# Kernel optimization log

Measured on AMD Instinct MI355X. Metric: run time of the kernel, lower is better.

## Reference

```python
import jax, jax.numpy as jnp
import numpy as np

DIM = 512
NUM_HEADS = 8
HEAD_DIM = DIM // NUM_HEADS


def setup_inputs() -> dict:
    key = jax.random.key(0)
    ks = jax.random.split(key, 5)
    s = 0.02
    x = jax.random.normal(ks[0], (2, 4096, DIM), dtype=jnp.float32)
    W_qkv = jax.random.normal(ks[1], (DIM, 3 * DIM), dtype=jnp.float32) * s
    b_qkv = jnp.zeros((3 * DIM,), dtype=jnp.float32)
    W_proj = jax.random.normal(ks[2], (DIM, DIM), dtype=jnp.float32) * s
    b_proj = jnp.zeros((DIM,), dtype=jnp.float32)
    return {"x": x, "W_qkv": W_qkv, "b_qkv": b_qkv, "W_proj": W_proj, "b_proj": b_proj}


def reference(x, W_qkv, b_qkv, W_proj, b_proj):
    B, N, C = x.shape
    # qkv: [B,N,3C] -> [3,B,H,N,Dh]
    qkv = (x @ W_qkv + b_qkv).reshape(B, N, 3, NUM_HEADS, HEAD_DIM)
    qkv = jnp.transpose(qkv, (2, 0, 3, 1, 4))
    q, k, v = qkv[0], qkv[1], qkv[2]
    scale = HEAD_DIM ** -0.5
    # naive full attention matrix [B,H,N,N] (faithful to source)
    attn = jnp.einsum('bhqd,bhkd->bhqk', q, k) * scale
    attn = jax.nn.softmax(attn, axis=-1)
    out = jnp.einsum('bhqk,bhkd->bhqd', attn, v)  # [B,H,N,Dh]
    out = jnp.transpose(out, (0, 2, 1, 3)).reshape(B, N, C)
    return out @ W_proj + b_proj
```

## Files before the change

kernel.cpp:

```cpp
#include <hip/hip_runtime.h>
#include <stdint.h>

typedef _Float16 f16;
typedef _Float16 f16x4 __attribute__((ext_vector_type(4)));
typedef _Float16 f16x8 __attribute__((ext_vector_type(8)));
typedef float f32x4 __attribute__((ext_vector_type(4)));
typedef float f32x16 __attribute__((ext_vector_type(16)));
typedef uint32_t u32;
typedef u32 u32x2 __attribute__((ext_vector_type(2)));
typedef u32 u32x4 __attribute__((ext_vector_type(4)));

#define NHEADS 8
#define DH 64
#define BATCH 2
#define SEQ 4096
#define CDIM 512
#define MTOT (BATCH * SEQ)
#define QSCALE 0.18033688011112042f

__device__ __forceinline__ void gload_lds16(const void* g, void* l) {
  __builtin_amdgcn_global_load_lds(
      (const __attribute__((address_space(1))) uint32_t*)g,
      (__attribute__((address_space(3))) uint32_t*)l, 16, 0, 0);
}

__device__ __forceinline__ u32 pk2(float a, float b) {
  auto h = __builtin_amdgcn_cvt_pkrtz(a, b);
  return __builtin_bit_cast(u32, h);
}

__device__ __forceinline__ void pl32swap(u32& a, u32& b) {
  asm volatile("v_permlane32_swap_b32 %0, %1" : "+v"(a), "+v"(b));
}

__device__ __forceinline__ void tr64(const float* __restrict__ src,
                                     f16* __restrict__ dst, int k0, int n0,
                                     int Ns, int Ks, f16* L) {
  const int t = threadIdx.x;
#pragma unroll
  for (int i = 0; i < 8; ++i) {
    int idx = (i * 256 + t) * 2;
    int r = idx >> 6, c = idx & 63;
    float2 v = *(const float2*)(src + (size_t)(k0 + r) * Ns + n0 + c);
    L[c * 66 + r] = (f16)v.x;
    L[(c + 1) * 66 + r] = (f16)v.y;
  }
  __syncthreads();
#pragma unroll
  for (int i = 0; i < 8; ++i) {
    int idx = (i * 256 + t) * 2;
    int r = idx >> 6, c = idx & 63;
    *(u32*)(dst + (size_t)(n0 + r) * Ks + k0 + c) = *(const u32*)(L + r * 66 + c);
  }
}

__global__ void prep(const float* __restrict__ x, f16* __restrict__ xb,
                     const float* __restrict__ Wqkv, f16* __restrict__ wqkvT,
                     const float* __restrict__ Wproj, f16* __restrict__ wprojT) {
  __shared__ f16 L[64 * 66];
  const int b = blockIdx.x;
  if (b < 4096) {
    int i = (b * 256 + (int)threadIdx.x) * 4;
    float4 v = *(const float4*)(x + i);
    f16x4 o = {(f16)v.x, (f16)v.y, (f16)v.z, (f16)v.w};
    *(f16x4*)(xb + i) = o;
  } else if (b < 4096 + 192) {
    int tw = b - 4096;
    int kt = tw / 24, nt = tw % 24;
    tr64(Wqkv, wqkvT, kt << 6, nt << 6, 1536, 512, L);
  } else {
    int tw = b - 4096 - 192;
    int kt = tw >> 3, nt = tw & 7;
    tr64(Wproj, wprojT, kt << 6, nt << 6, 512, 512, L);
  }
}

template <int MODE>
__global__ __launch_bounds__(256) void gemm_f16(
    const f16* __restrict__ A, const f16* __restrict__ Bt,
    const float* __restrict__ bias, int Ncols,
    f16* __restrict__ Qo, f16* __restrict__ Ko, f16* __restrict__ Vo,
    float* __restrict__ Fo) {
  const int K = CDIM;
  const int nTN = Ncols >> 7;
  const int cpx = gridDim.x >> 3;
  const int vb = (blockIdx.x & 7) * cpx + (blockIdx.x >> 3);
  const int bm = vb / nTN, bn = vb % nTN;
  const int M0 = bm << 7, N0 = bn << 7;
  __shared__ __align__(16) char ldsA[128 * 64 * 2];
  __shared__ __align__(16) char ldsB[128 * 64 * 2];
  const int t = threadIdx.x;
  const int w = t >> 6, lane = t & 63;
  const int wr = w >> 1, wc = w & 1;
  const int lm = lane & 15, lk = lane >> 4;
  f32x4 acc[4][4] = {};

  const int srow = t >> 3;
  const int sj = t & 7;

  for (int k0 = 0; k0 < K; k0 += 64) {
    __syncthreads();
#pragma unroll
    for (int q = 0; q < 4; ++q) {
      int row = (q << 5) + srow;
      int col = (sj ^ (row & 7)) << 3;
      gload_lds16(A + (size_t)(M0 + row) * K + k0 + col,
                  ldsA + ((q << 8) + (w << 6)) * 16);
      gload_lds16(Bt + (size_t)(N0 + row) * K + k0 + col,
                  ldsB + ((q << 8) + (w << 6)) * 16);
    }
    asm volatile("s_waitcnt vmcnt(0)" ::: "memory");
    __syncthreads();
#pragma unroll
    for (int h = 0; h < 2; ++h) {
      f16x8 af[4], bf[4];
#pragma unroll
      for (int mi = 0; mi < 4; ++mi) {
        int row = (wr << 6) + (mi << 4) + lm;
        int slot = ((h << 2) + lk) ^ (row & 7);
        af[mi] = *(const f16x8*)(ldsA + row * 128 + slot * 16);
      }
#pragma unroll
      for (int ni = 0; ni < 4; ++ni) {
        int row = (wc << 6) + (ni << 4) + lm;
        int slot = ((h << 2) + lk) ^ (row & 7);
        bf[ni] = *(const f16x8*)(ldsB + row * 128 + slot * 16);
      }
#pragma unroll
      for (int mi = 0; mi < 4; ++mi)
#pragma unroll
        for (int ni = 0; ni < 4; ++ni)
          acc[mi][ni] = __builtin_amdgcn_mfma_f32_16x16x32_f16(af[mi], bf[ni], acc[mi][ni], 0, 0, 0);
    }
  }

  const int cbase = N0 + (wc << 6);
  if (MODE == 0) {
    const int tsec = cbase >> 9;
    const int hh = (cbase & 511) >> 6;
#pragma unroll
    for (int mi = 0; mi < 4; ++mi)
#pragma unroll
      for (int ni = 0; ni < 4; ++ni) {
        int c = cbase + (ni << 4) + lm;
        int d = c & 63;
        float bv = bias[c];
        if (tsec == 2) {
          int m0 = M0 + (wr << 6) + (mi << 4) + (lk << 2);
          int bb = m0 >> 12, tok = m0 & 4095;
          f16x4 vv = {(f16)(acc[mi][ni][0] + bv), (f16)(acc[mi][ni][1] + bv),
                      (f16)(acc[mi][ni][2] + bv), (f16)(acc[mi][ni][3] + bv)};
          *(f16x4*)(Vo + ((size_t)(bb * NHEADS + hh) * DH + d) * SEQ + tok) = vv;
        } else {
#pragma unroll
          for (int r = 0; r < 4; ++r) {
            int m = M0 + (wr << 6) + (mi << 4) + (lk << 2) + r;
            float v = acc[mi][ni][r] + bv;
            int bb = m >> 12, tok = m & 4095;
            size_t bh = (size_t)bb * NHEADS + hh;
            if (tsec == 0) Qo[(bh * SEQ + tok) * DH + d] = (f16)(v * QSCALE);
            else           Ko[(bh * SEQ + tok) * DH + d] = (f16)v;
          }
        }
      }
  } else {
#pragma unroll
    for (int mi = 0; mi < 4; ++mi)
#pragma unroll
      for (int ni = 0; ni < 4; ++ni) {
        int c = cbase + (ni << 4) + lm;
        float bv = bias[c];
#pragma unroll
        for (int r = 0; r < 4; ++r) {
          int m = M0 + (wr << 6) + (mi << 4) + (lk << 2) + r;
          Fo[(size_t)m * CDIM + c] = acc[mi][ni][r] + bv;
        }
      }
  }
}

__global__ __launch_bounds__(256, 2) void attn_f16(
    const f16* __restrict__ Qw, const f16* __restrict__ Kw,
    const f16* __restrict__ Vw, f16* __restrict__ Ao) {
  const int vb = ((blockIdx.x & 7) << 6) + (blockIdx.x >> 3);
  const int bh = vb >> 5;
  const int qt = vb & 31;
  const int t = threadIdx.x, lane = t & 63;
  const int l31 = lane & 31, hi = lane >> 5;
  const int w = t >> 6;
  const int p = w & 1;
  const int wq = w >> 1;
  __shared__ __align__(16) char lds[65536];
  const int qbase = (qt << 7) + (wq << 6);
  const int qA = qbase + l31;
  const int qB = qbase + 32 + l31;
  const f16* QbA = Qw + ((size_t)bh * SEQ + qA) * DH;
  const f16* QbB = Qw + ((size_t)bh * SEQ + qB) * DH;
  f16x8 qfA[4], qfB[4];
#pragma unroll
  for (int cd = 0; cd < 4; ++cd) {
    qfA[cd] = *(const f16x8*)(QbA + cd * 16 + hi * 8);
    qfB[cd] = *(const f16x8*)(QbB + cd * 16 + hi * 8);
  }
  f32x16 oA0 = {}, oA1 = {}, oB0 = {}, oB1 = {};
  float lA = 0.f, lB = 0.f;
  const f16* Kb = Kw + (size_t)bh * SEQ * DH;
  const f16* Vb = Vw + (size_t)bh * DH * SEQ;
  const int srow = t >> 3, sj = t & 7;

#define STAGE(buf, kv0_)                                                      \
  {                                                                           \
    _Pragma("unroll") for (int q2 = 0; q2 < 2; ++q2) {                        \
      const int row = (q2 << 5) + srow;                                       \
      const int col = (sj ^ (row & 7)) << 3;                                  \
      gload_lds16(Kb + (size_t)((kv0_) + row) * DH + col,                     \
                  lds + (buf) * 16384 + row * 128 + sj * 16);                 \
      gload_lds16(Vb + (size_t)row * SEQ + (kv0_) + col,                      \
                  lds + 32768 + (buf) * 16384 + row * 128 + sj * 16);         \
    }                                                                         \
  }

  STAGE(0, 0);
  __syncthreads();

#pragma unroll 2
  for (int tt = 0; tt < 64; ++tt) {
    const int cur = tt & 1;
    const char* Kc = lds + cur * 16384;
    const char* Vc = lds + 32768 + cur * 16384;
    if (tt < 63) STAGE(cur ^ 1, (tt + 1) << 6);

    f16x8 kf[4];
    const int krow = (p << 5) + l31;
#pragma unroll
    for (int cd = 0; cd < 4; ++cd)
      kf[cd] = *(const f16x8*)(Kc + krow * 128 + ((((cd << 1) | hi) ^ (l31 & 7)) << 4));

    f32x16 sA = {}, sB = {};
#pragma unroll
    for (int cd = 0; cd < 4; ++cd) {
      sA = __builtin_amdgcn_mfma_f32_32x32x16_f16(kf[cd], qfA[cd], sA, 0, 0, 0);
      sB = __builtin_amdgcn_mfma_f32_32x32x16_f16(kf[cd], qfB[cd], sB, 0, 0, 0);
    }

    f16x8 pfA[2], pfB[2];
#define SOFTMAX(s, l, pf)                                                     \
    {                                                                         \
      _Pragma("unroll") for (int i = 0; i < 16; ++i)                          \
          s[i] = __builtin_amdgcn_exp2f(s[i]);                                \
      float a8[8];                                                            \
      _Pragma("unroll") for (int i = 0; i < 8; ++i) a8[i] = s[i] + s[i + 8];  \
      l += ((a8[0] + a8[1]) + (a8[2] + a8[3])) +                              \
           ((a8[4] + a8[5]) + (a8[6] + a8[7]));                               \
      _Pragma("unroll") for (int c = 0; c < 2; ++c) {                         \
        u32 a0 = pk2(s[8 * c + 0], s[8 * c + 1]);                             \
        u32 a1 = pk2(s[8 * c + 2], s[8 * c + 3]);                             \
        u32 b0 = pk2(s[8 * c + 4], s[8 * c + 5]);                             \
        u32 b1 = pk2(s[8 * c + 6], s[8 * c + 7]);                             \
        pl32swap(a0, b0);                                                     \
        pl32swap(a1, b1);                                                     \
        u32x4 pw = {a0, a1, b0, b1};                                          \
        pf[c] = __builtin_bit_cast(f16x8, pw);                                \
      }                                                                       \
    }
    SOFTMAX(sA, lA, pfA);
    SOFTMAX(sB, lB, pfB);

    f16x8 vf0[2], vf1[2];
#pragma unroll
    for (int c2 = 0; c2 < 2; ++c2) {
      const int ck = (p << 1) | c2;
      const int sl = (((ck << 1) | hi) ^ (l31 & 7)) << 4;
      vf0[c2] = *(const f16x8*)(Vc + l31 * 128 + sl);
      vf1[c2] = *(const f16x8*)(Vc + (32 + l31) * 128 + sl);
    }
#pragma unroll
    for (int c2 = 0; c2 < 2; ++c2) {
      oA0 = __builtin_amdgcn_mfma_f32_32x32x16_f16(vf0[c2], pfA[c2], oA0, 0, 0, 0);
      oA1 = __builtin_amdgcn_mfma_f32_32x32x16_f16(vf1[c2], pfA[c2], oA1, 0, 0, 0);
      oB0 = __builtin_amdgcn_mfma_f32_32x32x16_f16(vf0[c2], pfB[c2], oB0, 0, 0, 0);
      oB1 = __builtin_amdgcn_mfma_f32_32x32x16_f16(vf1[c2], pfB[c2], oB1, 0, 0, 0);
    }
    __syncthreads();
  }

  float* ob = (float*)(lds) + (((wq << 6) + lane) << 5);
  float* mlb = (float*)(lds + 16384) + ((wq << 6) + lane);
  const int b_ = bh >> 3, h_ = bh & 7;

#define MERGE_WRITE(o0, o1, l, myq)                                           \
    {                                                                         \
      if (p) {                                                                \
        *(f32x16*)ob = o0;                                                    \
        *(f32x16*)(ob + 16) = o1;                                             \
        mlb[0] = l;                                                           \
      }                                                                       \
      __syncthreads();                                                        \
      if (!p) {                                                               \
        f32x16 po0 = *(const f32x16*)ob;                                      \
        f32x16 po1 = *(const f32x16*)(ob + 16);                               \
        float lt = l + mlb[0];                                                \
        lt += __shfl_xor(lt, 32);                                             \
        float inv = 1.0f / lt;                                                \
        f16* orow = Ao + ((size_t)b_ * SEQ + (myq)) * CDIM + (h_ << 6) + (hi << 2); \
        _Pragma("unroll") for (int u = 0; u < 4; ++u) {                       \
          float e0 = (o0[4 * u] + po0[4 * u]) * inv;                          \
          float e1 = (o0[4 * u + 1] + po0[4 * u + 1]) * inv;                  \
          float e2 = (o0[4 * u + 2] + po0[4 * u + 2]) * inv;                  \
          float e3 = (o0[4 * u + 3] + po0[4 * u + 3]) * inv;                  \
          u32x2 pa = {pk2(e0, e1), pk2(e2, e3)};                              \
          *reinterpret_cast<u32x2*>(orow + (u << 3)) = pa;                    \
          float f0 = (o1[4 * u] + po1[4 * u]) * inv;                          \
          float f1 = (o1[4 * u + 1] + po1[4 * u + 1]) * inv;                  \
          float f2 = (o1[4 * u + 2] + po1[4 * u + 2]) * inv;                  \
          float f3 = (o1[4 * u + 3] + po1[4 * u + 3]) * inv;                  \
          u32x2 pb = {pk2(f0, f1), pk2(f2, f3)};                              \
          *reinterpret_cast<u32x2*>(orow + 32 + (u << 3)) = pb;               \
        }                                                                     \
      }                                                                       \
      __syncthreads();                                                        \
    }

  MERGE_WRITE(oA0, oA1, lA, qA);
  MERGE_WRITE(oB0, oB1, lB, qB);
}

extern "C" void kernel_launch(void* const* d_in, const int* in_sizes, int n_in,
                              void* d_out, int out_size, void* d_ws, size_t ws_size,
                              hipStream_t stream) {
  const float* x = (const float*)d_in[0];
  const float* Wqkv = (const float*)d_in[1];
  const float* bqkv = (const float*)d_in[2];
  const float* Wproj = (const float*)d_in[3];
  const float* bproj = (const float*)d_in[4];
  float* out = (float*)d_out;
  char* ws = (char*)d_ws;

  const size_t SZ_X = (size_t)MTOT * CDIM * 2;
  f16* xb = (f16*)(ws);
  f16* attno = xb;
  f16* wqkvT = (f16*)(ws + SZ_X);
  f16* wprojT = (f16*)(ws + SZ_X + (size_t)1536 * 512 * 2);
  f16* Qwv = (f16*)(ws + SZ_X + (size_t)1536 * 512 * 2 + (size_t)512 * 512 * 2);
  f16* Kwv = (f16*)((char*)Qwv + SZ_X);
  f16* Vwv = (f16*)((char*)Kwv + SZ_X);

  prep<<<4096 + 192 + 64, 256, 0, stream>>>(x, xb, Wqkv, wqkvT, Wproj, wprojT);
  gemm_f16<0><<<64 * 12, 256, 0, stream>>>(xb, wqkvT, bqkv, 1536, Qwv, Kwv, Vwv, nullptr);
  attn_f16<<<16 * 32, 256, 0, stream>>>(Qwv, Kwv, Vwv, attno);
  gemm_f16<1><<<64 * 4, 256, 0, stream>>>(attno, wprojT, bproj, 512, nullptr, nullptr, nullptr, out);
}
```

Measured before the change: 128.8 us.

## Triple-buffer K/V tiles with explicit vmcnt waits in attention loop

Replaces the double-buffered K/V LDS staging with a three-stage ring that prefetches two tiles ahead, using explicit s_waitcnt vmcnt counts plus a raw s_barrier instead of a full __syncthreads per iteration. The aim is to hide global-to-LDS load latency behind the MFMA/softmax work and avoid draining all outstanding loads each step. LDS use drops from 64KB to 48KB, which may help occupancy. The loop is no longer unrolled, and the vmcnt-based synchronization is fragile: it is only correct if exactly the expected number of loads are in flight.

```diff
diff --git a/kernel.cpp b/kernel.cpp
--- a/kernel.cpp
+++ b/kernel.cpp
@@ -190,7 +190,7 @@
   const int w = t >> 6;
   const int p = w & 1;
   const int wq = w >> 1;
-  __shared__ __align__(16) char lds[65536];
+  __shared__ __align__(16) char lds[49152];
   const int qbase = (qt << 7) + (wq << 6);
   const int qA = qbase + l31;
   const int qB = qbase + 32 + l31;
@@ -207,43 +207,20 @@
   const f16* Kb = Kw + (size_t)bh * SEQ * DH;
   const f16* Vb = Vw + (size_t)bh * DH * SEQ;
   const int srow = t >> 3, sj = t & 7;
-
-#define STAGE(buf, kv0_)                                                      \
+  const int krow = (p << 5) + l31;
+
+#define STAGE(Kst, Vst, kv0_)                                                 \
   {                                                                           \
     _Pragma("unroll") for (int q2 = 0; q2 < 2; ++q2) {                        \
       const int row = (q2 << 5) + srow;                                       \
       const int col = (sj ^ (row & 7)) << 3;                                  \
       gload_lds16(Kb + (size_t)((kv0_) + row) * DH + col,                     \
-                  lds + (buf) * 16384 + row * 128 + sj * 16);                 \
+                  (Kst) + row * 128 + sj * 16);                               \
       gload_lds16(Vb + (size_t)row * SEQ + (kv0_) + col,                      \
-                  lds + 32768 + (buf) * 16384 + row * 128 + sj * 16);         \
+                  (Vst) + row * 128 + sj * 16);                               \
     }                                                                         \
   }
 
-  STAGE(0, 0);
-  __syncthreads();
-
-#pragma unroll 2
-  for (int tt = 0; tt < 64; ++tt) {
-    const int cur = tt & 1;
-    const char* Kc = lds + cur * 16384;
-    const char* Vc = lds + 32768 + cur * 16384;
-    if (tt < 63) STAGE(cur ^ 1, (tt + 1) << 6);
-
-    f16x8 kf[4];
-    const int krow = (p << 5) + l31;
-#pragma unroll
-    for (int cd = 0; cd < 4; ++cd)
-      kf[cd] = *(const f16x8*)(Kc + krow * 128 + ((((cd << 1) | hi) ^ (l31 & 7)) << 4));
-
-    f32x16 sA = {}, sB = {};
-#pragma unroll
-    for (int cd = 0; cd < 4; ++cd) {
-      sA = __builtin_amdgcn_mfma_f32_32x32x16_f16(kf[cd], qfA[cd], sA, 0, 0, 0);
-      sB = __builtin_amdgcn_mfma_f32_32x32x16_f16(kf[cd], qfB[cd], sB, 0, 0, 0);
-    }
-
-    f16x8 pfA[2], pfB[2];
 #define SOFTMAX(s, l, pf)                                                     \
     {                                                                         \
       _Pragma("unroll") for (int i = 0; i < 16; ++i)                          \
@@ -263,27 +240,59 @@
         pf[c] = __builtin_bit_cast(f16x8, pw);                                \
       }                                                                       \
     }
-    SOFTMAX(sA, lA, pfA);
-    SOFTMAX(sB, lB, pfB);
-
-    f16x8 vf0[2], vf1[2];
-#pragma unroll
-    for (int c2 = 0; c2 < 2; ++c2) {
-      const int ck = (p << 1) | c2;
-      const int sl = (((ck << 1) | hi) ^ (l31 & 7)) << 4;
-      vf0[c2] = *(const f16x8*)(Vc + l31 * 128 + sl);
-      vf1[c2] = *(const f16x8*)(Vc + (32 + l31) * 128 + sl);
-    }
-#pragma unroll
-    for (int c2 = 0; c2 < 2; ++c2) {
-      oA0 = __builtin_amdgcn_mfma_f32_32x32x16_f16(vf0[c2], pfA[c2], oA0, 0, 0, 0);
-      oA1 = __builtin_amdgcn_mfma_f32_32x32x16_f16(vf1[c2], pfA[c2], oA1, 0, 0, 0);
-      oB0 = __builtin_amdgcn_mfma_f32_32x32x16_f16(vf0[c2], pfB[c2], oB0, 0, 0, 0);
-      oB1 = __builtin_amdgcn_mfma_f32_32x32x16_f16(vf1[c2], pfB[c2], oB1, 0, 0, 0);
-    }
-    __syncthreads();
-  }
-
+
+#define COMPUTE(Kc, Vc)                                                       \
+  {                                                                           \
+    f16x8 kf[4];                                                              \
+    _Pragma("unroll") for (int cd = 0; cd < 4; ++cd)                          \
+        kf[cd] = *(const f16x8*)((Kc) + krow * 128 +                          \
+                                 ((((cd << 1) | hi) ^ (l31 & 7)) << 4));      \
+    f32x16 sA = {}, sB = {};                                                  \
+    _Pragma("unroll") for (int cd = 0; cd < 4; ++cd) {                        \
+      sA = __builtin_amdgcn_mfma_f32_32x32x16_f16(kf[cd], qfA[cd], sA, 0, 0, 0); \
+      sB = __builtin_amdgcn_mfma_f32_32x32x16_f16(kf[cd], qfB[cd], sB, 0, 0, 0); \
+    }                                                                         \
+    f16x8 pfA[2], pfB[2];                                                     \
+    SOFTMAX(sA, lA, pfA);                                                     \
+    SOFTMAX(sB, lB, pfB);                                                     \
+    f16x8 vf0[2], vf1[2];                                                     \
+    _Pragma("unroll") for (int c2 = 0; c2 < 2; ++c2) {                        \
+      const int ck = (p << 1) | c2;                                           \
+      const int sl = (((ck << 1) | hi) ^ (l31 & 7)) << 4;                     \
+      vf0[c2] = *(const f16x8*)((Vc) + l31 * 128 + sl);                       \
+      vf1[c2] = *(const f16x8*)((Vc) + (32 + l31) * 128 + sl);                \
+    }                                                                         \
+    _Pragma("unroll") for (int c2 = 0; c2 < 2; ++c2) {                        \
+      oA0 = __builtin_amdgcn_mfma_f32_32x32x16_f16(vf0[c2], pfA[c2], oA0, 0, 0, 0); \
+      oA1 = __builtin_amdgcn_mfma_f32_32x32x16_f16(vf1[c2], pfA[c2], oA1, 0, 0, 0); \
+      oB0 = __builtin_amdgcn_mfma_f32_32x32x16_f16(vf0[c2], pfB[c2], oB0, 0, 0, 0); \
+      oB1 = __builtin_amdgcn_mfma_f32_32x32x16_f16(vf1[c2], pfB[c2], oB1, 0, 0, 0); \
+    }                                                                         \
+  }
+
+  char* K0 = lds;            char* V0 = lds + 24576;
+  char* K1 = lds + 8192;     char* V1 = lds + 32768;
+  char* K2 = lds + 16384;    char* V2 = lds + 40960;
+
+  STAGE(K0, V0, 0);
+  STAGE(K1, V1, 64);
+  char *Kc_ = K0, *Vc_ = V0, *Kn_ = K1, *Vn_ = V1, *Ks_ = K2, *Vs_ = V2;
+
+#pragma unroll 1
+  for (int tt = 0; tt < 64; ++tt) {
+    if (tt < 63) {
+      asm volatile("s_waitcnt vmcnt(8)" ::: "memory");
+    } else {
+      asm volatile("s_waitcnt vmcnt(0)" ::: "memory");
+    }
+    __builtin_amdgcn_s_barrier();
+    COMPUTE(Kc_, Vc_);
+    if (tt < 62) STAGE(Ks_, Vs_, (tt + 2) << 6);
+    char* tk = Kc_; Kc_ = Kn_; Kn_ = Ks_; Ks_ = tk;
+    char* tv = Vc_; Vc_ = Vn_; Vn_ = Vs_; Vs_ = tv;
+  }
+
+  __syncthreads();
   float* ob = (float*)(lds) + (((wq << 6) + lane) << 5);
   float* mlb = (float*)(lds + 16384) + ((wq << 6) + lane);
   const int b_ = bh >> 3, h_ = bh & 7;
```

Result: no change. 127.9 us (-0.7%).
